# Optimization experiments

Measured on AMD Instinct MI355X. Metric: run time of the kernel, lower is better.

Reference implementation:

```python
import jax, jax.numpy as jnp
import numpy as np

D, H, E, C, B = 1024, 2048, 8, 1024, 8192


def setup_inputs() -> dict:
    key = jax.random.key(0)
    ks = jax.random.split(key, 12)
    s_d = 1.0 / np.sqrt(D)
    s_h = 1.0 / np.sqrt(H)
    return {
        "x": jax.random.normal(ks[0], (B, D), dtype=jnp.float32),
        # gate (Router): Linear(D,D) -> relu -> Linear(D,E) -> softmax
        "gate_w1": jax.random.normal(ks[1], (D, D), dtype=jnp.float32) * s_d,
        "gate_b1": jax.random.normal(ks[2], (D,), dtype=jnp.float32) * s_d,
        "gate_w2": jax.random.normal(ks[3], (D, E), dtype=jnp.float32) * s_d,
        "gate_b2": jax.random.normal(ks[4], (E,), dtype=jnp.float32) * s_d,
        # experts stacked: fc1 [E,D,H], fc2 [E,H,H]
        "W1": jax.random.normal(ks[5], (E, D, H), dtype=jnp.float32) * s_d,
        "b1": jax.random.normal(ks[6], (E, H), dtype=jnp.float32) * s_d,
        "W2": jax.random.normal(ks[7], (E, H, H), dtype=jnp.float32) * s_h,
        "b2": jax.random.normal(ks[8], (E, H), dtype=jnp.float32) * s_h,
        # classifier Linear(H, C)
        "clf_w": jax.random.normal(ks[9], (H, C), dtype=jnp.float32) * s_h,
        "clf_b": jax.random.normal(ks[10], (C,), dtype=jnp.float32) * s_h,
    }


def reference(x, gate_w1, gate_b1, gate_w2, gate_b2, W1, b1, W2, b2, clf_w, clf_b):
    # Router: softmax over experts (dim=1)
    g = jax.nn.relu(x @ gate_w1 + gate_b1)          # [B, D]
    scores = jax.nn.softmax(g @ gate_w2 + gate_b2, axis=1)  # [B, E]

    # All experts, dense (training-mode forward): batched GEMMs over E
    h = jax.nn.relu(jnp.einsum('bd,edh->beh', x, W1) + b1[None])   # [B, E, H]
    expert_outs = jnp.einsum('beh,ehk->bek', h, W2) + b2[None]      # [B, E, H]

    # Shared classifier applied per (token, expert)
    logits = jnp.einsum('beh,hc->bec', expert_outs, clf_w) + clf_b  # [B, E, C]
    return logits, scores
```

## Files before the change

kernel.cpp:

```cpp
#include <hip/hip_runtime.h>
#include <stdint.h>

#define B_DIM 8192
#define D_DIM 1024
#define H_DIM 2048
#define E_DIM 8
#define C_DIM 1024

typedef _Float16 f16x8 __attribute__((ext_vector_type(8)));
typedef float f32x4 __attribute__((ext_vector_type(4)));

__device__ __forceinline__ void store_val(float* p, float v) { *p = v; }
__device__ __forceinline__ void store_val(_Float16* p, float v) { *p = (_Float16)v; }

__device__ __forceinline__ void async_cp16(const void* g, void* l) {
  __builtin_amdgcn_global_load_lds((const __attribute__((address_space(1))) void*)g,
                                   (__attribute__((address_space(3))) void*)l, 16, 0, 0);
}

template <bool RELU, bool BIAS, typename OUT_T>
__global__ void __launch_bounds__(256) gemm_bt(
    const _Float16* __restrict__ A, long aZ,
    const _Float16* __restrict__ Bt, long bZ,
    const float* __restrict__ bias, long biasZ,
    OUT_T* __restrict__ out, long outZ,
    int K, long rs)
{
  __shared__ _Float16 ldsA[128 * 64];
  __shared__ _Float16 ldsB[128 * 64];

  const int z = blockIdx.z;
  A   += (size_t)z * aZ;
  Bt  += (size_t)z * bZ;
  if (BIAS) bias += (size_t)z * biasZ;
  out += (size_t)z * outZ;

  const int tid  = threadIdx.x;
  const int wave = tid >> 6;
  const int lane = tid & 63;
  const int q    = lane >> 4;
  const int l16  = lane & 15;
  const int l8   = lane >> 3;
  const int l7   = lane & 7;

  const int m0   = blockIdx.y * 128;
  const int n0   = blockIdx.x * 128;
  const int wrow = (wave >> 1) * 64;
  const int wcol = (wave & 1) * 64;

  const int swz_st = ((l7 ^ l8) << 3);
  const _Float16* pa[4];
  const _Float16* pb[4];
#pragma unroll
  for (int i = 0; i < 4; ++i) {
    int ci = wave * 4 + i;
    pa[i] = A  + (size_t)(m0 + ci * 8 + l8) * K + swz_st;
    pb[i] = Bt + (size_t)(n0 + ci * 8 + l8) * K + swz_st;
  }

  int a_off[2][4], b_off[2][4];
#pragma unroll
  for (int kk = 0; kk < 2; ++kk) {
#pragma unroll
    for (int r = 0; r < 4; ++r) {
      int sw = ((kk * 4 + q) ^ (l16 & 7)) << 4;
      a_off[kk][r] = (wrow + r * 16 + l16) * 128 + sw;
      b_off[kk][r] = (wcol + r * 16 + l16) * 128 + sw;
    }
  }

  f32x4 acc[4][4];
#pragma unroll
  for (int r = 0; r < 4; ++r)
#pragma unroll
    for (int c = 0; c < 4; ++c)
      acc[r][c] = (f32x4){0.f, 0.f, 0.f, 0.f};

  const char* lAc = (const char*)ldsA;
  const char* lBc = (const char*)ldsB;

  for (int kt = 0; kt < K; kt += 64) {
    __syncthreads();
#pragma unroll
    for (int i = 0; i < 4; ++i) {
      int ci = wave * 4 + i;
      async_cp16(pa[i], ldsA + ci * 512);
      async_cp16(pb[i], ldsB + ci * 512);
      pa[i] += 64;
      pb[i] += 64;
    }
    __syncthreads();
#pragma unroll
    for (int kk = 0; kk < 2; ++kk) {
      f16x8 af[4], bfv[4];
#pragma unroll
      for (int r = 0; r < 4; ++r) af[r]  = *(const f16x8*)(lAc + a_off[kk][r]);
#pragma unroll
      for (int c = 0; c < 4; ++c) bfv[c] = *(const f16x8*)(lBc + b_off[kk][c]);
#pragma unroll
      for (int r = 0; r < 4; ++r)
#pragma unroll
        for (int c = 0; c < 4; ++c)
          acc[r][c] = __builtin_amdgcn_mfma_f32_16x16x32_f16(af[r], bfv[c], acc[r][c], 0, 0, 0);
    }
  }

#pragma unroll
  for (int c = 0; c < 4; ++c) {
    int col = n0 + wcol + c * 16 + l16;
    float bv = BIAS ? bias[col] : 0.f;
#pragma unroll
    for (int r = 0; r < 4; ++r) {
      int row = m0 + wrow + r * 16 + q * 4;
      f32x4 v = acc[r][c];
#pragma unroll
      for (int i = 0; i < 4; ++i) {
        float xv = v[i] + bv;
        if (RELU) xv = fmaxf(xv, 0.f);
        store_val(out + (size_t)(row + i) * rs + col, xv);
      }
    }
  }
}

template <bool RELU, bool BIAS, typename OUT_T, int K_CT>
__global__ void __launch_bounds__(512) gemm256(
    const _Float16* __restrict__ A, long aZ,
    const _Float16* __restrict__ Bt, long bZ,
    const float* __restrict__ bias, long biasZ,
    OUT_T* __restrict__ out, long outZ, long rs)
{
  constexpr int NT = K_CT / 64;
  __shared__ _Float16 ldsA[2 * 256 * 64];
  __shared__ _Float16 ldsB[2 * 256 * 64];

  const int z = blockIdx.z;
  A   += (size_t)z * aZ;
  Bt  += (size_t)z * bZ;
  if (BIAS) bias += (size_t)z * biasZ;
  out += (size_t)z * outZ;

  const int nwg = gridDim.x * gridDim.y;
  const int wg  = blockIdx.y * gridDim.x + blockIdx.x;
  const int sw  = (wg & 7) * (nwg >> 3) + (wg >> 3);
  const int bx  = sw % gridDim.x;
  const int by  = sw / gridDim.x;

  const int tid  = threadIdx.x;
  const int wave = tid >> 6;
  const int lane = tid & 63;
  const int q    = lane >> 4;
  const int l16  = lane & 15;
  const int l8   = lane >> 3;
  const int l7   = lane & 7;

  const int m0   = by * 256;
  const int n0   = bx * 256;
  const int wm   = wave >> 2;
  const int wn   = wave & 3;
  const int wrow = wm * 128;
  const int wcol = wn * 64;

  const int swz_st = ((l7 ^ l8) << 3);
  const _Float16* paB = A  + (size_t)(m0 + wave * 16 + l8) * K_CT + swz_st;
  const _Float16* pbB = Bt + (size_t)(n0 + wave * 16 + l8) * K_CT + swz_st;

  int a_base[2], b_base[2];
#pragma unroll
  for (int kk = 0; kk < 2; ++kk) {
    int swr = (((kk * 4 + q) ^ (l16 & 7)) << 4);
    a_base[kk] = (wrow + l16) * 128 + swr;
    b_base[kk] = (wcol + l16) * 128 + swr;
  }

  f32x4 acc[8][4];
#pragma unroll
  for (int r = 0; r < 8; ++r)
#pragma unroll
    for (int c = 0; c < 4; ++c)
      acc[r][c] = (f32x4){0.f, 0.f, 0.f, 0.f};

  const char* lA = (const char*)ldsA;
  const char* lB = (const char*)ldsB;

#define STAGE_A(bufe, hh, ptr)                                                        \
  {                                                                                   \
    _Pragma("unroll")                                                                 \
    for (int i_ = 0; i_ < 2; ++i_)                                                    \
      async_cp16((ptr) + (size_t)((hh) * 128 + i_ * 8) * K_CT,                        \
                 (void*)(ldsA + (bufe) + (hh) * 8192 + (wave * 2 + i_) * 512));       \
  }
#define STAGE_B(bufe, hh, ptr)                                                        \
  {                                                                                   \
    _Pragma("unroll")                                                                 \
    for (int i_ = 0; i_ < 2; ++i_)                                                    \
      async_cp16((ptr) + (size_t)((hh) * 128 + i_ * 8) * K_CT,                        \
                 (void*)(ldsB + (bufe) + (hh) * 8192 + (wave * 2 + i_) * 512));       \
  }

  STAGE_A(0, 0, paB) STAGE_A(0, 1, paB)
  STAGE_B(0, 0, pbB) STAGE_B(0, 1, pbB)
  STAGE_B(16384, 0, pbB + 64) STAGE_B(16384, 1, pbB + 64)
  asm volatile("s_waitcnt vmcnt(4)" ::: "memory");
  __builtin_amdgcn_s_barrier();

  const _Float16* pa_t = paB + 64;
  const _Float16* pb_t = pbB + 128;

  for (int t = 0; t < NT; ++t) {
    const int bofs  = (t & 1) * 32768;
    const int nbufe = ((t + 1) & 1) * 16384;
    const int cbufe = (t & 1) * 16384;
    f16x8 bf[4];
#pragma unroll
    for (int p = 0; p < 4; ++p) {
      const int kk = p >> 1, h = p & 1;
      if (h == 0) {
#pragma unroll
        for (int c = 0; c < 4; ++c)
          bf[c] = *(const f16x8*)(lB + bofs + b_base[kk] + c * 2048);
      }
      f16x8 af[4];
#pragma unroll
      for (int r = 0; r < 4; ++r)
        af[r] = *(const f16x8*)(lA + bofs + a_base[kk] + (h * 4 + r) * 2048);

      if (p == 0 && t + 1 < NT) STAGE_A(nbufe, 0, pa_t)
      if (p == 1 && t + 1 < NT) STAGE_A(nbufe, 1, pa_t)
      if (p == 3 && t + 2 < NT) { STAGE_B(cbufe, 0, pb_t) STAGE_B(cbufe, 1, pb_t) }

      __builtin_amdgcn_s_setprio(1);
#pragma unroll
      for (int c = 0; c < 4; ++c)
#pragma unroll
        for (int r = 0; r < 4; ++r)
          acc[h * 4 + r][c] = __builtin_amdgcn_mfma_f32_16x16x32_f16(
              af[r], bf[c], acc[h * 4 + r][c], 0, 0, 0);
      __builtin_amdgcn_s_setprio(0);

      if (p == 3) {
        if (t < NT - 2) asm volatile("s_waitcnt vmcnt(4) lgkmcnt(0)" ::: "memory");
        else            asm volatile("s_waitcnt vmcnt(0) lgkmcnt(0)" ::: "memory");
      } else {
        asm volatile("s_waitcnt lgkmcnt(0)" ::: "memory");
      }
      __builtin_amdgcn_s_barrier();
    }
    pa_t += 64;
    pb_t += 64;
  }
#undef STAGE_A
#undef STAGE_B

#pragma unroll
  for (int c = 0; c < 4; ++c) {
    int col = n0 + wcol + c * 16 + l16;
    float bv = BIAS ? bias[col] : 0.f;
#pragma unroll
    for (int r = 0; r < 8; ++r) {
      int row = m0 + wrow + r * 16 + q * 4;
      f32x4 v = acc[r][c];
#pragma unroll
      for (int i = 0; i < 4; ++i) {
        float xv = v[i] + bv;
        if (RELU) xv = fmaxf(xv, 0.f);
        store_val(out + (size_t)(row + i) * rs + col, xv);
      }
    }
  }
}

__global__ void cast_f32_f16(const float* __restrict__ in, _Float16* __restrict__ out, int n) {
  int i = (blockIdx.x * blockDim.x + threadIdx.x) * 4;
  if (i >= n) return;
  float4 v = *(const float4*)(in + i);
  union { _Float16 h[4]; uint2 u; } r;
  r.h[0] = (_Float16)v.x; r.h[1] = (_Float16)v.y;
  r.h[2] = (_Float16)v.z; r.h[3] = (_Float16)v.w;
  *(uint2*)(out + i) = r.u;
}

__global__ void transpose_cast(const float* __restrict__ in, _Float16* __restrict__ out,
                               int R, int Cn) {
  __shared__ float tile[32][33];
  in  += (size_t)blockIdx.z * R * Cn;
  out += (size_t)blockIdx.z * R * Cn;
  int c0 = blockIdx.x * 32, r0 = blockIdx.y * 32;
  int tx = threadIdx.x, ty = threadIdx.y;
#pragma unroll
  for (int i = ty; i < 32; i += 8)
    tile[i][tx] = in[(size_t)(r0 + i) * Cn + c0 + tx];
  __syncthreads();
#pragma unroll
  for (int i = ty; i < 32; i += 8)
    out[(size_t)(c0 + i) * R + r0 + tx] = (_Float16)tile[tx][i];
}

__global__ void gate2_softmax(const _Float16* __restrict__ g, const float* __restrict__ w2,
                              const float* __restrict__ b2, float* __restrict__ scores) {
  int b = blockIdx.x;
  int t = threadIdx.x;
  int e = t & 7, slice = t >> 3;
  const _Float16* gr = g + (size_t)b * D_DIM;
  float acc = 0.f;
  for (int d = slice; d < D_DIM; d += 32)
    acc += (float)gr[d] * w2[d * 8 + e];
  __shared__ float red[256];
  red[t] = acc;
  __syncthreads();
  for (int s = 16; s > 0; s >>= 1) {
    if (slice < s) red[t] += red[t + s * 8];
    __syncthreads();
  }
  __shared__ float sm[8];
  if (t < 8) sm[t] = red[t] + b2[t];
  __syncthreads();
  if (t == 0) {
    float mx = sm[0];
#pragma unroll
    for (int i = 1; i < 8; ++i) mx = fmaxf(mx, sm[i]);
    float ex[8], s = 0.f;
#pragma unroll
    for (int i = 0; i < 8; ++i) { ex[i] = expf(sm[i] - mx); s += ex[i]; }
    float inv = 1.f / s;
#pragma unroll
    for (int i = 0; i < 8; ++i) scores[(size_t)b * 8 + i] = ex[i] * inv;
  }
}

__global__ void combined_bias(const float* __restrict__ b2, const float* __restrict__ cw,
                              const float* __restrict__ cb, float* __restrict__ bc) {
  int e  = blockIdx.y;
  int cl = threadIdx.x & 63;
  int c  = blockIdx.x * 64 + cl;
  int ks = threadIdx.x >> 6;
  float acc = 0.f;
  for (int k = ks; k < H_DIM; k += 4)
    acc += b2[e * H_DIM + k] * cw[(size_t)k * C_DIM + c];
  __shared__ float red[256];
  red[threadIdx.x] = acc;
  __syncthreads();
  if (ks == 0)
    bc[(size_t)e * C_DIM + c] = red[cl] + red[cl + 64] + red[cl + 128] + red[cl + 192] + cb[c];
}

extern "C" void kernel_launch(void* const* d_in, const int* in_sizes, int n_in,
                              void* d_out, int out_size, void* d_ws, size_t ws_size,
                              hipStream_t stream) {
  const float* x   = (const float*)d_in[0];
  const float* gw1 = (const float*)d_in[1];
  const float* gb1 = (const float*)d_in[2];
  const float* gw2 = (const float*)d_in[3];
  const float* gb2 = (const float*)d_in[4];
  const float* W1  = (const float*)d_in[5];
  const float* b1  = (const float*)d_in[6];
  const float* W2  = (const float*)d_in[7];
  const float* b2  = (const float*)d_in[8];
  const float* cw  = (const float*)d_in[9];
  const float* cb  = (const float*)d_in[10];

  char* ws = (char*)d_ws;
  _Float16* xb     = (_Float16*)(ws);
  _Float16* g      = (_Float16*)(ws + 16777216ull);
  _Float16* gw1t   = (_Float16*)(ws + 33554432ull);
  _Float16* W1t    = (_Float16*)(ws + 35651584ull);
  _Float16* W2c    = (_Float16*)(ws + 69206016ull);
  _Float16* cwt    = (_Float16*)(ws + 136314880ull);
  _Float16* WcombT = (_Float16*)(ws + 140509184ull);
  float*    bc     = (float*)   (ws + 174063616ull);
  _Float16* h_all  = (_Float16*)(ws + 174096384ull);

  float* logits = (float*)d_out;
  float* scores = logits + (size_t)B_DIM * E_DIM * C_DIM;

  cast_f32_f16<<<B_DIM * D_DIM / 4 / 256, 256, 0, stream>>>(x, xb, B_DIM * D_DIM);
  transpose_cast<<<dim3(32, 32, 1), dim3(32, 8), 0, stream>>>(gw1, gw1t, D_DIM, D_DIM);
  transpose_cast<<<dim3(64, 32, 8), dim3(32, 8), 0, stream>>>(W1, W1t, D_DIM, H_DIM);
  cast_f32_f16<<<E_DIM * H_DIM * H_DIM / 4 / 256, 256, 0, stream>>>(W2, W2c, E_DIM * H_DIM * H_DIM);
  transpose_cast<<<dim3(32, 64, 1), dim3(32, 8), 0, stream>>>(cw, cwt, H_DIM, C_DIM);

  gemm_bt<true, true, _Float16><<<dim3(8, 64, 1), 256, 0, stream>>>(
      xb, 0, gw1t, 0, gb1, 0, g, 0, D_DIM, (long)D_DIM);
  gate2_softmax<<<B_DIM, 256, 0, stream>>>(g, gw2, gb2, scores);

  gemm256<false, false, _Float16, H_DIM><<<dim3(8, 4, 8), 512, 0, stream>>>(
      cwt, 0, W2c, (long)H_DIM * H_DIM, nullptr, 0,
      WcombT, (long)C_DIM * H_DIM, (long)H_DIM);
  combined_bias<<<dim3(C_DIM / 64, E_DIM), 256, 0, stream>>>(b2, cw, cb, bc);

  gemm256<true, true, _Float16, D_DIM><<<dim3(8, 32, 8), 512, 0, stream>>>(
      xb, 0, W1t, (long)H_DIM * D_DIM, b1, (long)H_DIM,
      h_all, (long)B_DIM * H_DIM, (long)H_DIM);

  gemm256<false, true, float, H_DIM><<<dim3(4, 32, 8), 512, 0, stream>>>(
      h_all, (long)B_DIM * H_DIM, WcombT, (long)C_DIM * H_DIM, bc, (long)C_DIM,
      logits, (long)C_DIM, (long)(E_DIM * C_DIM));
}
```

Measured before the change: 1.406 ms.

## Replace 256-tile GEMMs with double-buffered 128-tile GEMM and grouped block swizzle

Measured after the change: 1.631 ms. +16.0%, slower.

```diff
diff --git a/kernel.cpp b/kernel.cpp
--- a/kernel.cpp
+++ b/kernel.cpp
@@ -18,22 +18,28 @@
                                    (__attribute__((address_space(3))) void*)l, 16, 0, 0);
 }
 
-template <bool RELU, bool BIAS, typename OUT_T>
-__global__ void __launch_bounds__(256) gemm_bt(
+template <bool RELU, bool BIAS, typename OUT_T, int K_CT>
+__global__ void __launch_bounds__(256) gemm128(
     const _Float16* __restrict__ A, long aZ,
     const _Float16* __restrict__ Bt, long bZ,
     const float* __restrict__ bias, long biasZ,
-    OUT_T* __restrict__ out, long outZ,
-    int K, long rs)
+    OUT_T* __restrict__ out, long outZ, long rs)
 {
-  __shared__ _Float16 ldsA[128 * 64];
-  __shared__ _Float16 ldsB[128 * 64];
+  constexpr int NT = K_CT / 64;
+  __shared__ _Float16 ldsA[2 * 128 * 64];
+  __shared__ _Float16 ldsB[2 * 128 * 64];
 
   const int z = blockIdx.z;
   A   += (size_t)z * aZ;
   Bt  += (size_t)z * bZ;
   if (BIAS) bias += (size_t)z * biasZ;
   out += (size_t)z * outZ;
+
+  const int gx = gridDim.x;
+  const int w  = blockIdx.y * gx + blockIdx.x;
+  const int s  = w >> 3;
+  const int bx = s % gx;
+  const int by = (w & 7) + 8 * (s / gx);
 
   const int tid  = threadIdx.x;
   const int wave = tid >> 6;
@@ -43,8 +49,8 @@
   const int l8   = lane >> 3;
   const int l7   = lane & 7;
 
-  const int m0   = blockIdx.y * 128;
-  const int n0   = blockIdx.x * 128;
+  const int m0   = by * 128;
+  const int n0   = bx * 128;
   const int wrow = (wave >> 1) * 64;
   const int wcol = (wave & 1) * 64;
 
@@ -54,8 +60,8 @@
 #pragma unroll
   for (int i = 0; i < 4; ++i) {
     int ci = wave * 4 + i;
-    pa[i] = A  + (size_t)(m0 + ci * 8 + l8) * K + swz_st;
-    pb[i] = Bt + (size_t)(n0 + ci * 8 + l8) * K + swz_st;
+    pa[i] = A  + (size_t)(m0 + ci * 8 + l8) * K_CT + swz_st;
+    pb[i] = Bt + (size_t)(n0 + ci * 8 + l8) * K_CT + swz_st;
   }
 
   int a_off[2][4], b_off[2][4];
@@ -79,29 +85,70 @@
   const char* lAc = (const char*)ldsA;
   const char* lBc = (const char*)ldsB;
 
-  for (int kt = 0; kt < K; kt += 64) {
-    __syncthreads();
-#pragma unroll
-    for (int i = 0; i < 4; ++i) {
-      int ci = wave * 4 + i;
-      async_cp16(pa[i], ldsA + ci * 512);
-      async_cp16(pb[i], ldsB + ci * 512);
-      pa[i] += 64;
-      pb[i] += 64;
+#pragma unroll
+  for (int i = 0; i < 4; ++i) {
+    int ci = wave * 4 + i;
+    async_cp16(pa[i], ldsA + ci * 512);
+    async_cp16(pb[i], ldsB + ci * 512);
+    pa[i] += 64;
+    pb[i] += 64;
+  }
+  asm volatile("s_waitcnt vmcnt(0)" ::: "memory");
+  __builtin_amdgcn_s_barrier();
+
+  for (int t = 0; t < NT; ++t) {
+    const int bofs = (t & 1) * 16384;
+    const int nbuf = ((t + 1) & 1) * 8192;
+
+    {
+      f16x8 af[4], bfv[4];
+#pragma unroll
+      for (int r = 0; r < 4; ++r) af[r]  = *(const f16x8*)(lAc + bofs + a_off[0][r]);
+#pragma unroll
+      for (int c = 0; c < 4; ++c) bfv[c] = *(const f16x8*)(lBc + bofs + b_off[0][c]);
+      if (t + 1 < NT) {
+#pragma unroll
+        for (int i = 0; i < 4; ++i)
+          async_cp16(pa[i], ldsA + nbuf + (wave * 4 + i) * 512);
+      }
+      __builtin_amdgcn_s_barrier();
+      asm volatile("s_waitcnt lgkmcnt(0)" ::: "memory");
+      __builtin_amdgcn_sched_barrier(0);
+      __builtin_amdgcn_s_setprio(1);
+#pragma unroll
+      for (int c = 0; c < 4; ++c)
+#pragma unroll
+        for (int r = 0; r < 4; ++r)
+          acc[r][c] = __builtin_amdgcn_mfma_f32_16x16x32_f16(af[r], bfv[c], acc[r][c], 0, 0, 0);
+      __builtin_amdgcn_s_setprio(0);
+      __builtin_amdgcn_s_barrier();
     }
-    __syncthreads();
-#pragma unroll
-    for (int kk = 0; kk < 2; ++kk) {
+
+    {
       f16x8 af[4], bfv[4];
 #pragma unroll
-      for (int r = 0; r < 4; ++r) af[r]  = *(const f16x8*)(lAc + a_off[kk][r]);
-#pragma unroll
-      for (int c = 0; c < 4; ++c) bfv[c] = *(const f16x8*)(lBc + b_off[kk][c]);
-#pragma unroll
-      for (int r = 0; r < 4; ++r)
-#pragma unroll
-        for (int c = 0; c < 4; ++c)
+      for (int r = 0; r < 4; ++r) af[r]  = *(const f16x8*)(lAc + bofs + a_off[1][r]);
+#pragma unroll
+      for (int c = 0; c < 4; ++c) bfv[c] = *(const f16x8*)(lBc + bofs + b_off[1][c]);
+      if (t + 1 < NT) {
+#pragma unroll
+        for (int i = 0; i < 4; ++i)
+          async_cp16(pb[i], ldsB + nbuf + (wave * 4 + i) * 512);
+      }
+      __builtin_amdgcn_s_barrier();
+      asm volatile("s_waitcnt lgkmcnt(0)" ::: "memory");
+      __builtin_amdgcn_sched_barrier(0);
+      __builtin_amdgcn_s_setprio(1);
+#pragma unroll
+      for (int c = 0; c < 4; ++c)
+#pragma unroll
+        for (int r = 0; r < 4; ++r)
           acc[r][c] = __builtin_amdgcn_mfma_f32_16x16x32_f16(af[r], bfv[c], acc[r][c], 0, 0, 0);
+      __builtin_amdgcn_s_setprio(0);
+      asm volatile("s_waitcnt vmcnt(0)" ::: "memory");
+      __builtin_amdgcn_s_barrier();
+#pragma unroll
+      for (int i = 0; i < 4; ++i) { pa[i] += 64; pb[i] += 64; }
     }
   }
 
@@ -111,153 +158,6 @@
     float bv = BIAS ? bias[col] : 0.f;
 #pragma unroll
     for (int r = 0; r < 4; ++r) {
-      int row = m0 + wrow + r * 16 + q * 4;
-      f32x4 v = acc[r][c];
-#pragma unroll
-      for (int i = 0; i < 4; ++i) {
-        float xv = v[i] + bv;
-        if (RELU) xv = fmaxf(xv, 0.f);
-        store_val(out + (size_t)(row + i) * rs + col, xv);
-      }
-    }
-  }
-}
-
-template <bool RELU, bool BIAS, typename OUT_T, int K_CT>
-__global__ void __launch_bounds__(512) gemm256(
-    const _Float16* __restrict__ A, long aZ,
-    const _Float16* __restrict__ Bt, long bZ,
-    const float* __restrict__ bias, long biasZ,
-    OUT_T* __restrict__ out, long outZ, long rs)
-{
-  constexpr int NT = K_CT / 64;
-  __shared__ _Float16 ldsA[2 * 256 * 64];
-  __shared__ _Float16 ldsB[2 * 256 * 64];
-
-  const int z = blockIdx.z;
-  A   += (size_t)z * aZ;
-  Bt  += (size_t)z * bZ;
-  if (BIAS) bias += (size_t)z * biasZ;
-  out += (size_t)z * outZ;
-
-  const int nwg = gridDim.x * gridDim.y;
-  const int wg  = blockIdx.y * gridDim.x + blockIdx.x;
-  const int sw  = (wg & 7) * (nwg >> 3) + (wg >> 3);
-  const int bx  = sw % gridDim.x;
-  const int by  = sw / gridDim.x;
-
-  const int tid  = threadIdx.x;
-  const int wave = tid >> 6;
-  const int lane = tid & 63;
-  const int q    = lane >> 4;
-  const int l16  = lane & 15;
-  const int l8   = lane >> 3;
-  const int l7   = lane & 7;
-
-  const int m0   = by * 256;
-  const int n0   = bx * 256;
-  const int wm   = wave >> 2;
-  const int wn   = wave & 3;
-  const int wrow = wm * 128;
-  const int wcol = wn * 64;
-
-  const int swz_st = ((l7 ^ l8) << 3);
-  const _Float16* paB = A  + (size_t)(m0 + wave * 16 + l8) * K_CT + swz_st;
-  const _Float16* pbB = Bt + (size_t)(n0 + wave * 16 + l8) * K_CT + swz_st;
-
-  int a_base[2], b_base[2];
-#pragma unroll
-  for (int kk = 0; kk < 2; ++kk) {
-    int swr = (((kk * 4 + q) ^ (l16 & 7)) << 4);
-    a_base[kk] = (wrow + l16) * 128 + swr;
-    b_base[kk] = (wcol + l16) * 128 + swr;
-  }
-
-  f32x4 acc[8][4];
-#pragma unroll
-  for (int r = 0; r < 8; ++r)
-#pragma unroll
-    for (int c = 0; c < 4; ++c)
-      acc[r][c] = (f32x4){0.f, 0.f, 0.f, 0.f};
-
-  const char* lA = (const char*)ldsA;
-  const char* lB = (const char*)ldsB;
-
-#define STAGE_A(bufe, hh, ptr)                                                        \
-  {                                                                                   \
-    _Pragma("unroll")                                                                 \
-    for (int i_ = 0; i_ < 2; ++i_)                                                    \
-      async_cp16((ptr) + (size_t)((hh) * 128 + i_ * 8) * K_CT,                        \
-                 (void*)(ldsA + (bufe) + (hh) * 8192 + (wave * 2 + i_) * 512));       \
-  }
-#define STAGE_B(bufe, hh, ptr)                                                        \
-  {                                                                                   \
-    _Pragma("unroll")                                                                 \
-    for (int i_ = 0; i_ < 2; ++i_)                                                    \
-      async_cp16((ptr) + (size_t)((hh) * 128 + i_ * 8) * K_CT,                        \
-                 (void*)(ldsB + (bufe) + (hh) * 8192 + (wave * 2 + i_) * 512));       \
-  }
-
-  STAGE_A(0, 0, paB) STAGE_A(0, 1, paB)
-  STAGE_B(0, 0, pbB) STAGE_B(0, 1, pbB)
-  STAGE_B(16384, 0, pbB + 64) STAGE_B(16384, 1, pbB + 64)
-  asm volatile("s_waitcnt vmcnt(4)" ::: "memory");
-  __builtin_amdgcn_s_barrier();
-
-  const _Float16* pa_t = paB + 64;
-  const _Float16* pb_t = pbB + 128;
-
-  for (int t = 0; t < NT; ++t) {
-    const int bofs  = (t & 1) * 32768;
-    const int nbufe = ((t + 1) & 1) * 16384;
-    const int cbufe = (t & 1) * 16384;
-    f16x8 bf[4];
-#pragma unroll
-    for (int p = 0; p < 4; ++p) {
-      const int kk = p >> 1, h = p & 1;
-      if (h == 0) {
-#pragma unroll
-        for (int c = 0; c < 4; ++c)
-          bf[c] = *(const f16x8*)(lB + bofs + b_base[kk] + c * 2048);
-      }
-      f16x8 af[4];
-#pragma unroll
-      for (int r = 0; r < 4; ++r)
-        af[r] = *(const f16x8*)(lA + bofs + a_base[kk] + (h * 4 + r) * 2048);
-
-      if (p == 0 && t + 1 < NT) STAGE_A(nbufe, 0, pa_t)
-      if (p == 1 && t + 1 < NT) STAGE_A(nbufe, 1, pa_t)
-      if (p == 3 && t + 2 < NT) { STAGE_B(cbufe, 0, pb_t) STAGE_B(cbufe, 1, pb_t) }
-
-      __builtin_amdgcn_s_setprio(1);
-#pragma unroll
-      for (int c = 0; c < 4; ++c)
-#pragma unroll
-        for (int r = 0; r < 4; ++r)
-          acc[h * 4 + r][c] = __builtin_amdgcn_mfma_f32_16x16x32_f16(
-              af[r], bf[c], acc[h * 4 + r][c], 0, 0, 0);
-      __builtin_amdgcn_s_setprio(0);
-
-      if (p == 3) {
-        if (t < NT - 2) asm volatile("s_waitcnt vmcnt(4) lgkmcnt(0)" ::: "memory");
-        else            asm volatile("s_waitcnt vmcnt(0) lgkmcnt(0)" ::: "memory");
-      } else {
-        asm volatile("s_waitcnt lgkmcnt(0)" ::: "memory");
-      }
-      __builtin_amdgcn_s_barrier();
-    }
-    pa_t += 64;
-    pb_t += 64;
-  }
-#undef STAGE_A
-#undef STAGE_B
-
-#pragma unroll
-  for (int c = 0; c < 4; ++c) {
-    int col = n0 + wcol + c * 16 + l16;
-    float bv = BIAS ? bias[col] : 0.f;
-#pragma unroll
-    for (int r = 0; r < 8; ++r) {
       int row = m0 + wrow + r * 16 + q * 4;
       f32x4 v = acc[r][c];
 #pragma unroll
@@ -300,29 +200,33 @@
                               const float* __restrict__ b2, float* __restrict__ scores) {
   int b = blockIdx.x;
   int t = threadIdx.x;
-  int e = t & 7, slice = t >> 3;
+  int e = t >> 5, slice = t & 31;
   const _Float16* gr = g + (size_t)b * D_DIM;
   float acc = 0.f;
-  for (int d = slice; d < D_DIM; d += 32)
-    acc += (float)gr[d] * w2[d * 8 + e];
+  for (int d0 = slice * 8; d0 < D_DIM; d0 += 256) {
+    f16x8 gv = *(const f16x8*)(gr + d0);
+#pragma unroll
+    for (int j = 0; j < 8; ++j)
+      acc += (float)gv[j] * w2[(d0 + j) * 8 + e];
+  }
   __shared__ float red[256];
   red[t] = acc;
   __syncthreads();
-  for (int s = 16; s > 0; s >>= 1) {
-    if (slice < s) red[t] += red[t + s * 8];
+  for (int ss = 16; ss > 0; ss >>= 1) {
+    if (slice < ss) red[t] += red[t + ss];
     __syncthreads();
   }
   __shared__ float sm[8];
-  if (t < 8) sm[t] = red[t] + b2[t];
+  if (slice == 0) sm[e] = red[t] + b2[e];
   __syncthreads();
   if (t == 0) {
     float mx = sm[0];
 #pragma unroll
     for (int i = 1; i < 8; ++i) mx = fmaxf(mx, sm[i]);
-    float ex[8], s = 0.f;
-#pragma unroll
-    for (int i = 0; i < 8; ++i) { ex[i] = expf(sm[i] - mx); s += ex[i]; }
-    float inv = 1.f / s;
+    float ex[8], sum = 0.f;
+#pragma unroll
+    for (int i = 0; i < 8; ++i) { ex[i] = expf(sm[i] - mx); sum += ex[i]; }
+    float inv = 1.f / sum;
 #pragma unroll
     for (int i = 0; i < 8; ++i) scores[(size_t)b * 8 + i] = ex[i] * inv;
   }
@@ -379,20 +283,20 @@
   cast_f32_f16<<<E_DIM * H_DIM * H_DIM / 4 / 256, 256, 0, stream>>>(W2, W2c, E_DIM * H_DIM * H_DIM);
   transpose_cast<<<dim3(32, 64, 1), dim3(32, 8), 0, stream>>>(cw, cwt, H_DIM, C_DIM);
 
-  gemm_bt<true, true, _Float16><<<dim3(8, 64, 1), 256, 0, stream>>>(
-      xb, 0, gw1t, 0, gb1, 0, g, 0, D_DIM, (long)D_DIM);
+  gemm128<true, true, _Float16, D_DIM><<<dim3(8, 64, 1), 256, 0, stream>>>(
+      xb, 0, gw1t, 0, gb1, 0, g, 0, (long)D_DIM);
   gate2_softmax<<<B_DIM, 256, 0, stream>>>(g, gw2, gb2, scores);
 
-  gemm256<false, false, _Float16, H_DIM><<<dim3(8, 4, 8), 512, 0, stream>>>(
+  gemm128<false, false, _Float16, H_DIM><<<dim3(16, 8, 8), 256, 0, stream>>>(
       cwt, 0, W2c, (long)H_DIM * H_DIM, nullptr, 0,
       WcombT, (long)C_DIM * H_DIM, (long)H_DIM);
   combined_bias<<<dim3(C_DIM / 64, E_DIM), 256, 0, stream>>>(b2, cw, cb, bc);
 
-  gemm256<true, true, _Float16, D_DIM><<<dim3(8, 32, 8), 512, 0, stream>>>(
+  gemm128<true, true, _Float16, D_DIM><<<dim3(16, 64, 8), 256, 0, stream>>>(
       xb, 0, W1t, (long)H_DIM * D_DIM, b1, (long)H_DIM,
       h_all, (long)B_DIM * H_DIM, (long)H_DIM);
 
-  gemm256<false, true, float, H_DIM><<<dim3(4, 32, 8), 512, 0, stream>>>(
+  gemm128<false, true, float, H_DIM><<<dim3(8, 64, 8), 256, 0, stream>>>(
       h_all, (long)B_DIM * H_DIM, WcombT, (long)C_DIM * H_DIM, bc, (long)C_DIM,
       logits, (long)C_DIM, (long)(E_DIM * C_DIM));
 }
```
